# Performance work log

Hardware: AMD Instinct MI355X
Metric: run time of the kernel (lower is better)

Reference implementation:

```python
import jax, jax.numpy as jnp
import numpy as np

C, G = 512, 16            # channels, groups
GC = C // G               # group channels = 32
OFFSET_SCALE = 1.0
EPS = 1e-6


def setup_inputs() -> dict:
    key = jax.random.key(0)
    ks = jax.random.split(key, 4)
    N, H, W = 8, 64, 64
    return {
        "input_first": jax.random.normal(ks[0], (N, C, H, W), jnp.float32),
        "input_last": jax.random.normal(ks[1], (N, H, W, C), jnp.float32),
        "dw_w": jax.random.normal(ks[2], (C, 1, 3, 3), jnp.float32) * 0.1,  # depthwise kernel (OIHW, I=1)
        "dw_b": jnp.zeros((C,), jnp.float32),
        "ln_g": jnp.ones((C,), jnp.float32),
        "ln_b": jnp.zeros((C,), jnp.float32),
        "off_w": jax.random.normal(ks[3], (2 * G, C), jnp.float32) * 0.02,  # nonzero (module zero-inits)
        "off_b": jnp.zeros((2 * G,), jnp.float32),
    }


def _bilinear(img, px, py):
    # align_corners=False, padding_mode='zeros'.
    Hin, Win, _ = img.shape
    x0 = jnp.floor(px)
    y0 = jnp.floor(py)
    wx1 = px - x0
    wy1 = py - y0

    def tap(xi, yi, w):
        xc = jnp.clip(xi, 0, Win - 1).astype(jnp.int32)
        yc = jnp.clip(yi, 0, Hin - 1).astype(jnp.int32)
        valid = ((xi >= 0) & (xi <= Win - 1) & (yi >= 0) & (yi <= Hin - 1)).astype(img.dtype)
        return img[yc, xc] * (w * valid)[:, None]  # [L, GC]

    return (tap(x0, y0, (1 - wx1) * (1 - wy1)) + tap(x0 + 1, y0, wx1 * (1 - wy1)) +
            tap(x0, y0 + 1, (1 - wx1) * wy1) + tap(x0 + 1, y0 + 1, wx1 * wy1))


_sampler = jax.vmap(jax.vmap(_bilinear))  # over [N, G, ...]


def _forward(input_first, input_last, dw_w, dw_b, ln_g, ln_b, off_w, off_b):
    N, _, H, W = input_first.shape
    # --- dw_conv: depthwise 3x3 conv (pad 1) -> LN (channels_last) -> GELU ---
    x = jax.lax.conv_general_dilated(
        input_first, dw_w, window_strides=(1, 1), padding='SAME',
        dimension_numbers=('NCHW', 'OIHW', 'NCHW'), feature_group_count=C)
    x = x + dw_b[None, :, None, None]
    x = jnp.transpose(x, (0, 2, 3, 1))  # NHWC
    mu = x.mean(-1, keepdims=True)
    var = x.var(-1, keepdims=True)
    x1 = (x - mu) * jax.lax.rsqrt(var + EPS) * ln_g + ln_b
    x1 = jax.nn.gelu(x1, approximate=False)

    # --- offset prediction: [N,H,W, G*2], pairs are (x, y) per DCNv3 layout ---
    off = jnp.einsum('nhwc,oc->nhwo', x1, off_w) + off_b
    off = off.reshape(N, H, W, G, 2)

    # --- DCNv3 core, kernel_size=1, pad=0, stride=1, dilation=1 ---
    # ref point = pixel center; normalized loc = (i+0.5)/size + off*scale/size;
    # grid_sample pixel coord = loc*size - 0.5 = i + off*scale.
    px = jnp.arange(W, dtype=x1.dtype)[None, None, :, None] + off[..., 0] * OFFSET_SCALE  # [N,H,W,G]
    py = jnp.arange(H, dtype=x1.dtype)[None, :, None, None] + off[..., 1] * OFFSET_SCALE
    px = px.transpose(0, 3, 1, 2).reshape(N, G, H * W)
    py = py.transpose(0, 3, 1, 2).reshape(N, G, H * W)

    img = input_last.reshape(N, H, W, G, GC).transpose(0, 3, 1, 2, 4)  # [N,G,H,W,GC]
    sampled = _sampler(img, px, py)  # [N,G,HW,GC]

    mask = jnp.ones((N, G, H * W, 1), dtype=input_last.dtype)  # mask_dcn = ones
    out = (sampled * mask).reshape(N, G, H, W, GC)
    out = out.transpose(0, 2, 3, 1, 4).reshape(N, H, W, C)
    return jnp.transpose(out, (0, 3, 1, 2))  # NCHW, as in module's final permute


def reference(input_first, input_last, dw_w, dw_b, ln_g, ln_b, off_w, off_b):
    return _forward(input_first, input_last, dw_w, dw_b, ln_g, ln_b, off_w, off_b)
```

## Files before the change

kernel.cpp:

```cpp
#include <hip/hip_runtime.h>
#include <hip/hip_bf16.h>
#include <math.h>

#define NB 8
#define CC 512
#define HH 64
#define WW 64
#define GG 16
#define GCH 32
#define OO 32
#define NGHW (NB * GG * HH * WW)
#define NPX  (NB * HH * WW)
#define XROW 520


__device__ __forceinline__ float gelu_exact(float x) {
    return 0.5f * x * (1.0f + erff(x * 0.70710678118654752f));
}

__device__ __forceinline__ unsigned pack_bf2(float a, float b) {
    __hip_bfloat162 t = __float22bfloat162_rn(make_float2(a, b));
    return *(unsigned*)&t;
}

typedef __attribute__((ext_vector_type(8))) short bf16x8;
typedef __attribute__((ext_vector_type(4))) float f32x4;

__global__ __launch_bounds__(1024, 4)
void fused_conv_ln_gelu_off_kernel(const float* __restrict__ in_first,
                                   const float* __restrict__ dw_w,
                                   const float* __restrict__ dw_b,
                                   const float* __restrict__ ln_g,
                                   const float* __restrict__ ln_b,
                                   const float* __restrict__ off_w,
                                   const float* __restrict__ off_b,
                                   float* __restrict__ coords)
{
    const int h    = blockIdx.x;
    const int n    = blockIdx.y;
    const int tid  = threadIdx.x;
    const int wq   = tid & 31;
    const int cgrp = tid >> 5;
    const int wb   = wq * 2;
    const int c0   = cgrp * 16;
    const int wave = tid >> 6;
    const int lane = tid & 63;

    __shared__ short xbuf[64 * XROW];
    __shared__ float redS [16 * 64];
    __shared__ float redS2[16 * 64];
    __shared__ float mu_s[64];
    __shared__ float rs_s[64];

    float xv[2][16];
    float sw0 = 0.f, sw1 = 0.f, sq0 = 0.f, sq1 = 0.f;

    const float* inbase = in_first + (size_t)(n * CC + c0) * HH * WW;

    #pragma unroll
    for (int i = 0; i < 16; ++i) {
        const int c = c0 + i;
        float w9[9];
        #pragma unroll
        for (int k = 0; k < 9; ++k) w9[k] = dw_w[c * 9 + k];
        const float b = dw_b[c];
        float a0 = b, a1 = b;
        #pragma unroll
        for (int r = 0; r < 3; ++r) {
            const int y = h + r - 1;
            if (y < 0 || y >= HH) continue;
            const float2 m = *(const float2*)(inbase + ((size_t)i * HH + y) * WW + wb);
            float left  = __shfl_up(m.y, 1);
            float right = __shfl_down(m.x, 1);
            if (wq == 0)  left  = 0.0f;
            if (wq == 31) right = 0.0f;
            const float k0 = w9[r * 3 + 0], k1 = w9[r * 3 + 1], k2 = w9[r * 3 + 2];
            a0 += k0 * left + k1 * m.x + k2 * m.y;
            a1 += k0 * m.x  + k1 * m.y + k2 * right;
        }
        xv[0][i] = a0; xv[1][i] = a1;
        sw0 += a0; sq0 += a0 * a0;
        sw1 += a1; sq1 += a1 * a1;
    }

    sw0 += __shfl_xor(sw0, 32); sq0 += __shfl_xor(sq0, 32);
    sw1 += __shfl_xor(sw1, 32); sq1 += __shfl_xor(sq1, 32);
    if (lane < 32) {
        redS [wave * 64 + wb + 0] = sw0;  redS2[wave * 64 + wb + 0] = sq0;
        redS [wave * 64 + wb + 1] = sw1;  redS2[wave * 64 + wb + 1] = sq1;
    }
    __syncthreads();
    if (tid < 64) {
        float s = 0.f, s2 = 0.f;
        #pragma unroll
        for (int k = 0; k < 16; ++k) {
            s  += redS [k * 64 + tid];
            s2 += redS2[k * 64 + tid];
        }
        const float mu  = s * (1.0f / 512.0f);
        const float var = s2 * (1.0f / 512.0f) - mu * mu;
        mu_s[tid] = mu;
        rs_s[tid] = rsqrtf(var + 1e-6f);
    }
    __syncthreads();

    {
        const float mu0 = mu_s[wb + 0], rs0 = rs_s[wb + 0];
        const float mu1 = mu_s[wb + 1], rs1 = rs_s[wb + 1];
        unsigned pk0[8], pk1[8];
        #pragma unroll
        for (int t = 0; t < 8; ++t) {
            const int c = c0 + 2 * t;
            const float lgA = ln_g[c],     lbA = ln_b[c];
            const float lgB = ln_g[c + 1], lbB = ln_b[c + 1];
            const float v0a = (xv[0][2 * t]     - mu0) * rs0 * lgA + lbA;
            const float v0b = (xv[0][2 * t + 1] - mu0) * rs0 * lgB + lbB;
            const float v1a = (xv[1][2 * t]     - mu1) * rs1 * lgA + lbA;
            const float v1b = (xv[1][2 * t + 1] - mu1) * rs1 * lgB + lbB;
            pk0[t] = pack_bf2(gelu_exact(v0a), gelu_exact(v0b));
            pk1[t] = pack_bf2(gelu_exact(v1a), gelu_exact(v1b));
        }
        short* p0 = xbuf + (wb + 0) * XROW + c0;
        short* p1 = xbuf + (wb + 1) * XROW + c0;
        *(uint4*)(p0)     = make_uint4(pk0[0], pk0[1], pk0[2], pk0[3]);
        *(uint4*)(p0 + 8) = make_uint4(pk0[4], pk0[5], pk0[6], pk0[7]);
        *(uint4*)(p1)     = make_uint4(pk1[0], pk1[1], pk1[2], pk1[3]);
        *(uint4*)(p1 + 8) = make_uint4(pk1[4], pk1[5], pk1[6], pk1[7]);
    }
    __syncthreads();

    if (wave < 8) {
        const int ml   = lane & 15;
        const int quad = lane >> 4;
        const int pxT  = wave >> 1;
        const int oT   = wave & 1;

        const short* arow = xbuf + (pxT * 16 + ml) * XROW + quad * 8;
        const float* brow = off_w + (size_t)(oT * 16 + ml) * CC + quad * 8;

        f32x4 acc = {0.f, 0.f, 0.f, 0.f};
        for (int k = 0; k < CC; k += 32) {
            const bf16x8 af = *(const bf16x8*)(arow + k);
            const float4 p = *(const float4*)(brow + k);
            const float4 q = *(const float4*)(brow + k + 4);
            union { bf16x8 v; unsigned u[4]; } bb;
            bb.u[0] = pack_bf2(p.x, p.y); bb.u[1] = pack_bf2(p.z, p.w);
            bb.u[2] = pack_bf2(q.x, q.y); bb.u[3] = pack_bf2(q.z, q.w);
            acc = __builtin_amdgcn_mfma_f32_16x16x32_bf16(af, bb.v, acc, 0, 0, 0);
        }

        const int   o   = oT * 16 + ml;
        const float ob  = off_b[o];
        const int   par = o & 1;
        const int   g   = o >> 1;
        #pragma unroll
        for (int r = 0; r < 4; ++r) {
            const int w = pxT * 16 + quad * 4 + r;
            const float base = par ? (float)h : (float)w;
            coords[(size_t)par * NGHW + (((size_t)n * GG + g) * HH + h) * WW + w]
                = base + acc[r] + ob;
        }
    }
}

__global__ __launch_bounds__(256)
void sample_kernel(const float* __restrict__ in_last,
                   const float* __restrict__ coord_ws,
                   float* __restrict__ out)
{
    const int h   = blockIdx.x;
    const int n   = blockIdx.y;
    const int g   = blockIdx.z;
    const int tid = threadIdx.x;

    __shared__ float pxs[64];
    __shared__ float pys[64];
    __shared__ float smem[64 * 33];

    if (tid < 128) {
        const int w = tid & 63;
        const size_t cidx = (((size_t)n * GG + g) * HH + h) * WW + w;
        if (tid < 64) pxs[w] = coord_ws[cidx];
        else          pys[w] = coord_ws[cidx + NGHW];
    }
    __syncthreads();

    const int c4    = tid & 7;
    const int wslot = tid >> 3;
    const float* base = in_last + (size_t)n * HH * WW * CC + g * GCH + c4 * 4;

    #pragma unroll
    for (int pass = 0; pass < 2; ++pass) {
        const int w = wslot + pass * 32;
        const float px = pxs[w];
        const float py = pys[w];
        const float x0f = floorf(px), y0f = floorf(py);
        const float fx = px - x0f, fy = py - y0f;
        const int x0 = (int)x0f, y0 = (int)y0f;

        float4 acc = make_float4(0.f, 0.f, 0.f, 0.f);
        #pragma unroll
        for (int t = 0; t < 4; ++t) {
            const int xi = x0 + (t & 1);
            const int yi = y0 + (t >> 1);
            const float wt = ((t & 1) ? fx : 1.0f - fx) * ((t >> 1) ? fy : 1.0f - fy);
            if (xi >= 0 && xi < WW && yi >= 0 && yi < HH) {
                const float4 v = *(const float4*)(base + ((size_t)yi * WW + xi) * CC);
                acc.x += wt * v.x;
                acc.y += wt * v.y;
                acc.z += wt * v.z;
                acc.w += wt * v.w;
            }
        }
        float* sp = smem + w * 33 + c4 * 4;
        sp[0] = acc.x; sp[1] = acc.y; sp[2] = acc.z; sp[3] = acc.w;
    }
    __syncthreads();

    const int w  = tid & 63;
    const int cb = tid >> 6;
    float* op = out + (((size_t)n * CC + g * GCH) * HH + h) * WW + w;
    #pragma unroll
    for (int pass = 0; pass < 8; ++pass) {
        const int c = pass * 4 + cb;
        op[(size_t)c * (HH * WW)] = smem[w * 33 + c];
    }
}

extern "C" void kernel_launch(void* const* d_in, const int* in_sizes, int n_in,
                              void* d_out, int out_size, void* d_ws, size_t ws_size,
                              hipStream_t stream) {
    const float* in_first = (const float*)d_in[0];
    const float* in_last  = (const float*)d_in[1];
    const float* dw_w     = (const float*)d_in[2];
    const float* dw_b     = (const float*)d_in[3];
    const float* ln_g     = (const float*)d_in[4];
    const float* ln_b     = (const float*)d_in[5];
    const float* off_w    = (const float*)d_in[6];
    const float* off_b    = (const float*)d_in[7];
    float* out = (float*)d_out;

    float* coord_ws = (float*)d_ws;

    dim3 gridA(HH, NB);
    fused_conv_ln_gelu_off_kernel<<<gridA, 1024, 0, stream>>>(
        in_first, dw_w, dw_b, ln_g, ln_b, off_w, off_b, coord_ws);

    dim3 gridB(HH, NB, GG);
    sample_kernel<<<gridB, 256, 0, stream>>>(in_last, coord_ws, out);
}
```

Before: 282.7 us.

## Batch bilinear gathers, vectorize nontemporal stores, swizzle sample blocks, alias reduction smem

The sample kernel now computes all eight tap offsets and weights first, using clamped indices and zeroed weights for out-of-range taps, so it can issue all eight float4 gathers before accumulating. This raises memory-level parallelism in place of branchy, serialized loads. Output is written as float4 nontemporal stores over four consecutive w positions instead of scalar stores. The grid is flattened and block IDs are swizzled by a factor of 8, likely to spread blocks across XCDs. In the first kernel, the reduction scratch now aliases the xbuf shared array to cut LDS use, which could raise occupancy.

```diff
diff --git a/kernel.cpp b/kernel.cpp
--- a/kernel.cpp
+++ b/kernel.cpp
@@ -47,15 +47,15 @@
     const int lane = tid & 63;
 
     __shared__ short xbuf[64 * XROW];
-    __shared__ float redS [16 * 64];
-    __shared__ float redS2[16 * 64];
     __shared__ float mu_s[64];
     __shared__ float rs_s[64];
+    float* redS  = (float*)xbuf;
+    float* redS2 = (float*)xbuf + 1024;
 
     float xv[2][16];
     float sw0 = 0.f, sw1 = 0.f, sq0 = 0.f, sq1 = 0.f;
 
-    const float* inbase = in_first + (size_t)(n * CC + c0) * HH * WW;
+    const float* inbase = in_first + ((size_t)n * CC + c0) * HH * WW;
 
     #pragma unroll
     for (int i = 0; i < 16; ++i) {
@@ -120,8 +120,8 @@
             pk0[t] = pack_bf2(gelu_exact(v0a), gelu_exact(v0b));
             pk1[t] = pack_bf2(gelu_exact(v1a), gelu_exact(v1b));
         }
-        short* p0 = xbuf + (wb + 0) * XROW + c0;
-        short* p1 = xbuf + (wb + 1) * XROW + c0;
+        short* p0 = xbuf + (size_t)(wb + 0) * XROW + c0;
+        short* p1 = xbuf + (size_t)(wb + 1) * XROW + c0;
         *(uint4*)(p0)     = make_uint4(pk0[0], pk0[1], pk0[2], pk0[3]);
         *(uint4*)(p0 + 8) = make_uint4(pk0[4], pk0[5], pk0[6], pk0[7]);
         *(uint4*)(p1)     = make_uint4(pk1[0], pk1[1], pk1[2], pk1[3]);
@@ -135,7 +135,7 @@
         const int pxT  = wave >> 1;
         const int oT   = wave & 1;
 
-        const short* arow = xbuf + (pxT * 16 + ml) * XROW + quad * 8;
+        const short* arow = xbuf + (size_t)(pxT * 16 + ml) * XROW + quad * 8;
         const float* brow = off_w + (size_t)(oT * 16 + ml) * CC + quad * 8;
 
         f32x4 acc = {0.f, 0.f, 0.f, 0.f};
@@ -168,9 +168,11 @@
                    const float* __restrict__ coord_ws,
                    float* __restrict__ out)
 {
-    const int h   = blockIdx.x;
-    const int n   = blockIdx.y;
-    const int g   = blockIdx.z;
+    const int bid = blockIdx.x;
+    const int nb  = (bid & 7) * 1024 + (bid >> 3);
+    const int h   = nb & 63;
+    const int n   = (nb >> 6) & 7;
+    const int g   = nb >> 9;
     const int tid = threadIdx.x;
 
     __shared__ float pxs[64];
@@ -189,41 +191,60 @@
     const int wslot = tid >> 3;
     const float* base = in_last + (size_t)n * HH * WW * CC + g * GCH + c4 * 4;
 
-    #pragma unroll
-    for (int pass = 0; pass < 2; ++pass) {
-        const int w = wslot + pass * 32;
+    int   off[8];
+    float wt [8];
+    #pragma unroll
+    for (int p = 0; p < 2; ++p) {
+        const int w = wslot + p * 32;
         const float px = pxs[w];
         const float py = pys[w];
         const float x0f = floorf(px), y0f = floorf(py);
         const float fx = px - x0f, fy = py - y0f;
         const int x0 = (int)x0f, y0 = (int)y0f;
-
-        float4 acc = make_float4(0.f, 0.f, 0.f, 0.f);
         #pragma unroll
         for (int t = 0; t < 4; ++t) {
             const int xi = x0 + (t & 1);
             const int yi = y0 + (t >> 1);
-            const float wt = ((t & 1) ? fx : 1.0f - fx) * ((t >> 1) ? fy : 1.0f - fy);
-            if (xi >= 0 && xi < WW && yi >= 0 && yi < HH) {
-                const float4 v = *(const float4*)(base + ((size_t)yi * WW + xi) * CC);
-                acc.x += wt * v.x;
-                acc.y += wt * v.y;
-                acc.z += wt * v.z;
-                acc.w += wt * v.w;
-            }
-        }
-        float* sp = smem + w * 33 + c4 * 4;
-        sp[0] = acc.x; sp[1] = acc.y; sp[2] = acc.z; sp[3] = acc.w;
-    }
-    __syncthreads();
-
-    const int w  = tid & 63;
-    const int cb = tid >> 6;
-    float* op = out + (((size_t)n * CC + g * GCH) * HH + h) * WW + w;
-    #pragma unroll
-    for (int pass = 0; pass < 8; ++pass) {
-        const int c = pass * 4 + cb;
-        op[(size_t)c * (HH * WW)] = smem[w * 33 + c];
+            const int xc = min(max(xi, 0), WW - 1);
+            const int yc = min(max(yi, 0), HH - 1);
+            const float valid = (xi >= 0 && xi < WW && yi >= 0 && yi < HH) ? 1.0f : 0.0f;
+            wt [p * 4 + t] = ((t & 1) ? fx : 1.0f - fx) * ((t >> 1) ? fy : 1.0f - fy) * valid;
+            off[p * 4 + t] = (yc * WW + xc) * CC;
+        }
+    }
+    float4 v[8];
+    #pragma unroll
+    for (int i = 0; i < 8; ++i) v[i] = *(const float4*)(base + off[i]);
+
+    float4 a0 = make_float4(0.f, 0.f, 0.f, 0.f);
+    float4 a1 = make_float4(0.f, 0.f, 0.f, 0.f);
+    #pragma unroll
+    for (int t = 0; t < 4; ++t) {
+        a0.x += wt[t] * v[t].x;     a0.y += wt[t] * v[t].y;
+        a0.z += wt[t] * v[t].z;     a0.w += wt[t] * v[t].w;
+        a1.x += wt[4 + t] * v[4 + t].x; a1.y += wt[4 + t] * v[4 + t].y;
+        a1.z += wt[4 + t] * v[4 + t].z; a1.w += wt[4 + t] * v[4 + t].w;
+    }
+    {
+        float* sp0 = smem + wslot * 33 + c4 * 4;
+        float* sp1 = smem + (wslot + 32) * 33 + c4 * 4;
+        sp0[0] = a0.x; sp0[1] = a0.y; sp0[2] = a0.z; sp0[3] = a0.w;
+        sp1[0] = a1.x; sp1[1] = a1.y; sp1[2] = a1.z; sp1[3] = a1.w;
+    }
+    __syncthreads();
+
+    const int c  = tid >> 4;
+    const int w4 = (tid & 15) * 4;
+    #pragma unroll
+    for (int p = 0; p < 2; ++p) {
+        const int cc = c + p * 16;
+        f32x4 o;
+        o.x = smem[(w4 + 0) * 33 + cc];
+        o.y = smem[(w4 + 1) * 33 + cc];
+        o.z = smem[(w4 + 2) * 33 + cc];
+        o.w = smem[(w4 + 3) * 33 + cc];
+        __builtin_nontemporal_store(
+            o, (f32x4*)(out + (((size_t)n * CC + g * GCH + cc) * HH + h) * WW + w4));
     }
 }
 
@@ -246,6 +267,5 @@
     fused_conv_ln_gelu_off_kernel<<<gridA, 1024, 0, stream>>>(
         in_first, dw_w, dw_b, ln_g, ln_b, off_w, off_b, coord_ws);
 
-    dim3 gridB(HH, NB, GG);
-    sample_kernel<<<gridB, 256, 0, stream>>>(in_last, coord_ws, out);
-}
+    sample_kernel<<<HH * NB * GG, 256, 0, stream>>>(in_last, coord_ws, out);
+}
```

Result: faster. 269.7 us (-4.6%).
